# Kernel tuning notes

Measured on AMD Instinct MI355X. Metric: run time of the kernel, lower is better.

Reference implementation:

```python
import jax, jax.numpy as jnp
import numpy as np

T, N, I, H, OUT = 16, 4096, 4, 32, 1


def setup_inputs() -> dict:
    key = jax.random.key(0)
    ks = jax.random.split(key, 12)
    f32 = jnp.float32
    x_path = jax.random.normal(ks[0], (T, N, I), f32)
    adj = jax.random.normal(ks[1], (N, N), f32) / np.float32(np.sqrt(N))
    W_enc = jax.random.normal(ks[2], (I, H), f32) / np.float32(np.sqrt(I))
    b_enc = jnp.zeros((H,), f32)
    W_gcn = jax.random.normal(ks[3], (H, H), f32) / np.float32(np.sqrt(H))
    b_gcn = jnp.zeros((H,), f32)
    W_time = jax.random.normal(ks[4], (H, H), f32) / np.float32(np.sqrt(H))
    b_time = jnp.zeros((H,), f32)
    W_proj = jax.random.normal(ks[5], (H, H * I), f32) * np.float32(0.1 / np.sqrt(H))
    b_proj = jnp.zeros((H * I,), f32)
    W_d1 = jax.random.normal(ks[6], (H, 16), f32) / np.float32(np.sqrt(H))
    b_d1 = jnp.zeros((16,), f32)
    W_d2 = jax.random.normal(ks[7], (16, OUT), f32) / np.float32(4.0)
    b_d2 = jnp.zeros((OUT,), f32)
    return dict(x_path=x_path, adj=adj, W_enc=W_enc, b_enc=b_enc,
                W_gcn=W_gcn, b_gcn=b_gcn, W_time=W_time, b_time=b_time,
                W_proj=W_proj, b_proj=b_proj, W_d1=W_d1, b_d1=b_d1,
                W_d2=W_d2, b_d2=b_d2)


def _natural_cubic_coeffs(y):
    # y: (T, C) samples on uniform grid t=0..T-1 (h=1).
    # Natural cubic spline: tridiagonal solve for second derivatives M.
    Tn = y.shape[0]
    main = jnp.ones((Tn,), y.dtype).at[1:-1].set(4.0)
    A = jnp.diag(main)
    idx = jnp.arange(1, Tn - 1)
    A = A.at[idx, idx - 1].set(1.0).at[idx, idx + 1].set(1.0)
    rhs = jnp.zeros_like(y).at[1:-1].set(6.0 * (y[2:] - 2.0 * y[1:-1] + y[:-2]))
    M = jnp.linalg.solve(A, rhs)
    b = (y[1:] - y[:-1]) - (2.0 * M[:-1] + M[1:]) / 6.0
    c = M[:-1] / 2.0
    d = (M[1:] - M[:-1]) / 6.0
    return b, c, d  # each (T-1, C); dX/dt on interval i at local s: b+2cs+3ds^2


def reference(x_path, adj, W_enc, b_enc, W_gcn, b_gcn, W_time, b_time,
              W_proj, b_proj, W_d1, b_d1, W_d2, b_d2):
    Tn, Nn, In = x_path.shape
    Hn = W_enc.shape[1]
    y = x_path.reshape(Tn, Nn * In)
    sb, sc, sd = _natural_cubic_coeffs(y)

    # z0 = encoder(X(t0)); spline value at grid point 0 equals the sample.
    z0 = x_path[0] @ W_enc + b_enc  # (N, H)

    def vf(z, dxdt):
        # SpatialVectorField + projector + block-diagonal Jacobian applied to dX/dt.
        # z: (N, H), dxdt: (N, I)
        zn = adj @ z                                     # GCN neighbor aggregation
        h = jax.nn.relu(zn @ W_gcn + b_gcn + z @ W_time + b_time)
        sens = (h @ W_proj + b_proj).reshape(Nn, Hn, In)  # per-site Jacobian blocks
        # site_identity * sens -> block-diag; matmul with dX reduces to per-site contraction
        return jnp.einsum('nhi,ni->nh', sens, dxdt)

    def rk4_step(z, coefs):
        bi, ci, di = coefs  # (N*I,)
        def dxdt(s):
            return (bi + 2.0 * ci * s + 3.0 * di * s * s).reshape(Nn, In)
        k1 = vf(z, dxdt(0.0))
        k2 = vf(z + 0.5 * k1, dxdt(0.5))
        k3 = vf(z + 0.5 * k2, dxdt(0.5))
        k4 = vf(z + k3, dxdt(1.0))
        zn = z + (k1 + 2.0 * k2 + 2.0 * k3 + k4) / 6.0
        return zn, zn

    _, zs = jax.lax.scan(rk4_step, z0, (sb, sc, sd))
    zT = jnp.concatenate([z0[None], zs], axis=0)  # (T, N, H)

    hdec = jax.nn.relu(zT @ W_d1 + b_d1)
    return jax.nn.sigmoid(hdec @ W_d2 + b_d2)  # (T, N, OUT)
```

## Files before the change

### kernel.cpp

```cpp
#include <hip/hip_runtime.h>
#include <hip/hip_bf16.h>

#define NN 4096
#define NI 16384
#define HH 32

typedef __attribute__((ext_vector_type(8))) short short8;
typedef __attribute__((ext_vector_type(4))) float f32x4;

__device__ __forceinline__ short f2bs(float f) {
  __hip_bfloat16 b = __float2bfloat16(f);
  return *(short*)&b;
}

__global__ __launch_bounds__(512) void k_cvt(const float* __restrict__ a,
                                             short* __restrict__ ab) {
  const int tid = threadIdx.x;
  const int W = tid >> 6, lane = tid & 63;
  const int fr = lane & 15, oct = lane >> 4;
  const int R = blockIdx.x;
  const float* srow = a + (long)(R * 16 + fr) * NN + W * 512 + oct * 8;
  short* drow = ab + ((long)(R * 8 + W) * 16) * 512 + lane * 8;
#pragma unroll 4
  for (int i = 0; i < 16; ++i) {
    const float4 u0 = *(const float4*)(srow + i * 32);
    const float4 u1 = *(const float4*)(srow + i * 32 + 4);
    short8 r;
    r[0] = f2bs(u0.x); r[1] = f2bs(u0.y); r[2] = f2bs(u0.z); r[3] = f2bs(u0.w);
    r[4] = f2bs(u1.x); r[5] = f2bs(u1.y); r[6] = f2bs(u1.z); r[7] = f2bs(u1.w);
    *(short8*)(drow + i * 512) = r;
  }
}

__device__ __forceinline__ long zt_idx(int n, int h) {
  const int hb = h >> 4, hl = h & 15;
  const int kb = n >> 5, oct = (n >> 3) & 3, j = n & 7;
  return ((long)(hb * 128 + kb) * 64 + hl + 16 * oct) * 8 + j;
}

__global__ void k_spline(const float* __restrict__ x,
                         float* __restrict__ dx0, float* __restrict__ dxh,
                         float* __restrict__ dx1) {
  const int c = blockIdx.x * 256 + threadIdx.x;
  float y[16];
#pragma unroll
  for (int t = 0; t < 16; ++t) y[t] = x[t * NI + c];
  float cp[15], dp[15], M[16];
  cp[1] = 0.25f;
  dp[1] = (6.f * (y[2] - 2.f * y[1] + y[0])) * 0.25f;
#pragma unroll
  for (int i = 2; i <= 14; ++i) {
    float ri = 6.f * (y[i + 1] - 2.f * y[i] + y[i - 1]);
    float inv = 1.f / (4.f - cp[i - 1]);
    cp[i] = inv;
    dp[i] = (ri - dp[i - 1]) * inv;
  }
  M[0] = 0.f; M[15] = 0.f;
  M[14] = dp[14];
#pragma unroll
  for (int i = 13; i >= 1; --i) M[i] = dp[i] - cp[i] * M[i + 1];
#pragma unroll
  for (int i = 0; i < 15; ++i) {
    float b = (y[i + 1] - y[i]) - (2.f * M[i] + M[i + 1]) * (1.f / 6.f);
    float cc = 0.5f * M[i];
    float dd = (M[i + 1] - M[i]) * (1.f / 6.f);
    dx0[i * NI + c] = b;
    dxh[i * NI + c] = b + cc + 0.75f * dd;
    dx1[i * NI + c] = b + 2.f * cc + 3.f * dd;
  }
}

__global__ void k_enc(const float* __restrict__ x,
                      const float* __restrict__ We,
                      const float* __restrict__ be,
                      float* __restrict__ zcur, float* __restrict__ ze,
                      short* __restrict__ zT) {
  const int g = blockIdx.x * 256 + threadIdx.x;
  const int n = g >> 5, h = g & 31;
  float acc = be[h];
#pragma unroll
  for (int i = 0; i < 4; ++i) acc = fmaf(x[n * 4 + i], We[i * 32 + h], acc);
  zcur[g] = acc;
  ze[g] = acc;
  zT[zt_idx(n, h)] = f2bs(acc);
}

__global__ void k_dec0(const float* __restrict__ z,
                       const float* __restrict__ W1,
                       const float* __restrict__ b1,
                       const float* __restrict__ W2,
                       const float* __restrict__ b2,
                       float* __restrict__ out) {
  __shared__ float W1s[32][17];
  __shared__ float b1s[16], W2s[16], b2s;
  const int tid = threadIdx.x;
  for (int idx = tid; idx < 512; idx += 256) W1s[idx >> 4][idx & 15] = W1[idx];
  if (tid < 16) { b1s[tid] = b1[tid]; W2s[tid] = W2[tid]; }
  if (tid == 0) b2s = b2[0];
  __syncthreads();
  const int n = blockIdx.x * 256 + tid;
  const float* zr = z + (long)n * 32;
  float zv[32];
#pragma unroll
  for (int hh = 0; hh < 32; ++hh) zv[hh] = zr[hh];
  float acc = b2s;
#pragma unroll
  for (int jj = 0; jj < 16; ++jj) {
    float hv = b1s[jj];
#pragma unroll
    for (int hh = 0; hh < 32; ++hh) hv = fmaf(zv[hh], W1s[hh][jj], hv);
    acc = fmaf(fmaxf(hv, 0.f), W2s[jj], acc);
  }
  out[n] = 1.f / (1.f + expf(-acc));
}

__global__ __launch_bounds__(1024) void k_vf(
    const short* __restrict__ adjb,
    const short* __restrict__ zT_in,
    short* __restrict__ zT_out,
    float* __restrict__ z_eval,
    const float* __restrict__ z_base,
    float* __restrict__ z_next,
    float* __restrict__ kout,
    const float* __restrict__ k1, const float* __restrict__ k2,
    const float* __restrict__ k3,
    const float* __restrict__ dxsel,
    const float* __restrict__ Wg, const float* __restrict__ bg,
    const float* __restrict__ Wt, const float* __restrict__ bt,
    const float* __restrict__ Wp, const float* __restrict__ bp,
    const float* __restrict__ Wd1, const float* __restrict__ bd1,
    const float* __restrict__ Wd2, const float* __restrict__ bd2,
    float* __restrict__ out, int out_base, int j) {
  __shared__ float red2[16][32][17];
  __shared__ float zn_s[16][33];
  __shared__ float h_s[16][33];
  __shared__ float ze_s[16][33];
  __shared__ float Wg_s[32][32];
  __shared__ float Wt_s[32][32];
  __shared__ float Wp_s[32][136];
  __shared__ float Wd1_s[32][16];
  __shared__ float bgt_s[32];
  __shared__ float bp_s[128];
  __shared__ float dsm[33];

  const int tid = threadIdx.x;
  const int lane = tid & 63;
  const int w = tid >> 6;
  const int r0 = blockIdx.x * 16;
  const int lane8 = lane * 8;

  f32x4 a0 = {0.f,0.f,0.f,0.f}, a1 = {0.f,0.f,0.f,0.f};
  const short* ap  = adjb + ((long)(blockIdx.x * 128 + w * 8)) * 512 + lane8;
  const short* b0p = zT_in + ((long)(w * 8)) * 512 + lane8;
  const short* b1p = zT_in + ((long)(128 + w * 8)) * 512 + lane8;
#pragma unroll
  for (int i = 0; i < 8; ++i) {
    const short8 av = *(const short8*)(ap + i * 512);
    const short8 b0 = *(const short8*)(b0p + i * 512);
    const short8 b1 = *(const short8*)(b1p + i * 512);
    a0 = __builtin_amdgcn_mfma_f32_16x16x32_bf16(av, b0, a0, 0, 0, 0);
    a1 = __builtin_amdgcn_mfma_f32_16x16x32_bf16(av, b1, a1, 0, 0, 0);
  }

  for (int idx = tid; idx < 1024; idx += 1024) { }
  if (tid < 1024) {
    if (tid < 512) {
      Wg_s[tid >> 5][tid & 31] = Wg[tid];
      Wt_s[tid >> 5][tid & 31] = Wt[tid];
    } else {
      const int q = tid - 512;
      Wg_s[(q + 512) >> 5][q & 31] = Wg[512 + q];
      Wt_s[(q + 512) >> 5][q & 31] = Wt[512 + q];
    }
  }
  for (int idx = tid; idx < 4096; idx += 1024)
    Wp_s[idx >> 7][idx & 127] = Wp[idx];
  if (tid < 512) Wd1_s[tid >> 4][tid & 15] = Wd1[tid];
  if (tid < 32) bgt_s[tid] = bg[tid] + bt[tid];
  if (tid < 128) bp_s[tid] = bp[tid];
  if (tid < 512) ze_s[tid >> 5][tid & 31] = z_eval[r0 * 32 + tid];
  if (tid < 16) { dsm[tid] = bd1[tid]; dsm[16 + tid] = Wd2[tid]; }
  if (tid == 0) dsm[32] = bd2[0];

  {
    const int crow = (lane >> 4) * 4;
    const int ccol = lane & 15;
#pragma unroll
    for (int q = 0; q < 4; ++q) {
      red2[crow + q][ccol][w] = a0[q];
      red2[crow + q][ccol + 16][w] = a1[q];
    }
  }
  __syncthreads();

  const int r = (tid >> 5) & 15, c = tid & 31;
  if (tid < 512) {
    float zn = 0.f;
#pragma unroll
    for (int q = 0; q < 16; ++q) zn += red2[r][c][q];
    zn_s[r][c] = zn;
  }
  __syncthreads();

  if (tid < 512) {
    float hv = bgt_s[c];
#pragma unroll
    for (int kk = 0; kk < 32; ++kk)
      hv = fmaf(zn_s[r][kk], Wg_s[kk][c], fmaf(ze_s[r][kk], Wt_s[kk][c], hv));
    h_s[r][c] = fmaxf(hv, 0.f);
  }
  __syncthreads();

  float znew = 0.f;
  if (tid < 512) {
    const int row = r0 + r;
    float hr[32];
#pragma unroll
    for (int hp = 0; hp < 32; ++hp) hr[hp] = h_s[r][hp];
    float s0 = bp_s[c * 4], s1 = bp_s[c * 4 + 1], s2 = bp_s[c * 4 + 2], s3 = bp_s[c * 4 + 3];
#pragma unroll
    for (int hp = 0; hp < 32; ++hp) {
      const float4 wv = *(const float4*)&Wp_s[hp][c * 4];
      s0 = fmaf(hr[hp], wv.x, s0);
      s1 = fmaf(hr[hp], wv.y, s1);
      s2 = fmaf(hr[hp], wv.z, s2);
      s3 = fmaf(hr[hp], wv.w, s3);
    }
    const float4 dxv = *(const float4*)&dxsel[row * 4];
    const float kv = s0 * dxv.x + s1 * dxv.y + s2 * dxv.z + s3 * dxv.w;
    const long g = (long)row * 32 + c;
    if (j == 4) {
      znew = z_base[g] + (k1[g] + 2.f * k2[g] + 2.f * k3[g] + kv) * (1.f / 6.f);
      z_next[g] = znew;
    } else {
      kout[g] = kv;
      znew = z_base[g] + ((j == 3) ? 1.f : 0.5f) * kv;
    }
    z_eval[g] = znew;
    zT_out[zt_idx(row, c)] = f2bs(znew);
  }

  if (j == 4) {
    __syncthreads();
    if (tid < 512) zn_s[r][c] = znew;
    __syncthreads();
    if (tid < 16) {
      float acc = dsm[32];
#pragma unroll
      for (int jj = 0; jj < 16; ++jj) {
        float hv = dsm[jj];
#pragma unroll
        for (int hh = 0; hh < 32; ++hh) hv = fmaf(zn_s[tid][hh], Wd1_s[hh][jj], hv);
        acc = fmaf(fmaxf(hv, 0.f), dsm[16 + jj], acc);
      }
      out[out_base + r0 + tid] = 1.f / (1.f + expf(-acc));
    }
  }
}

extern "C" void kernel_launch(void* const* d_in, const int* in_sizes, int n_in,
                              void* d_out, int out_size, void* d_ws, size_t ws_size,
                              hipStream_t stream) {
  (void)in_sizes; (void)n_in; (void)out_size; (void)ws_size;
  const float* x      = (const float*)d_in[0];
  const float* adj    = (const float*)d_in[1];
  const float* W_enc  = (const float*)d_in[2];
  const float* b_enc  = (const float*)d_in[3];
  const float* W_gcn  = (const float*)d_in[4];
  const float* b_gcn  = (const float*)d_in[5];
  const float* W_time = (const float*)d_in[6];
  const float* b_time = (const float*)d_in[7];
  const float* W_proj = (const float*)d_in[8];
  const float* b_proj = (const float*)d_in[9];
  const float* W_d1   = (const float*)d_in[10];
  const float* b_d1   = (const float*)d_in[11];
  const float* W_d2   = (const float*)d_in[12];
  const float* b_d2   = (const float*)d_in[13];
  float* out = (float*)d_out;

  float* dx0   = (float*)d_ws;
  float* dxh   = dx0 + 15 * NI;
  float* dx1   = dxh + 15 * NI;
  float* zcur  = dx1 + 15 * NI;
  float* znext = zcur + NN * HH;
  float* zev   = znext + NN * HH;
  float* k1b   = zev + NN * HH;
  float* k2b   = k1b + NN * HH;
  float* k3b   = k2b + NN * HH;
  short* zTa   = (short*)(k3b + NN * HH);
  short* zTb   = zTa + HH * NN;
  short* adjb  = zTb + HH * NN;

  k_cvt<<<256, 512, 0, stream>>>(adj, adjb);
  k_spline<<<64, 256, 0, stream>>>(x, dx0, dxh, dx1);
  k_enc<<<512, 256, 0, stream>>>(x, W_enc, b_enc, zcur, zev, zTa);
  k_dec0<<<16, 256, 0, stream>>>(zcur, W_d1, b_d1, W_d2, b_d2, out);

  short* zin = zTa;
  short* zout = zTb;
  for (int t = 0; t < 15; ++t) {
    const float* ds[4] = { dx0 + t * NI, dxh + t * NI, dxh + t * NI, dx1 + t * NI };
    for (int j = 1; j <= 4; ++j) {
      float* ko = (j == 1) ? k1b : (j == 2) ? k2b : k3b;
      k_vf<<<256, 1024, 0, stream>>>(adjb, zin, zout, zev, zcur, znext, ko,
                                     k1b, k2b, k3b, ds[j - 1],
                                     W_gcn, b_gcn, W_time, b_time, W_proj, b_proj,
                                     W_d1, b_d1, W_d2, b_d2, out, (t + 1) * NN, j);
      short* tmp = zin; zin = zout; zout = tmp;
    }
    float* tz = zcur; zcur = znext; znext = tz;
  }
}
```

Measured before the change: 791.7 us.

## Fuse the whole RK4 integration into one persistent cooperative kernel with grid barriers

Replaces the 60 per-stage kernel launches, plus the separate convert, encoder and decoder kernels, with one persistent cooperative kernel. It synchronises the stages with a two-level atomic grid barrier. Each block keeps its bf16 slice of adj in registers, converted once from fp32, and holds z and the k accumulators in shared memory, so global round-trips of z, k1-k3 and the adj re-reads go away. The cost is a grid barrier per stage, higher register pressure from the 8 resident short8 fragments, and reliance on all 256 blocks being co-resident. If the cooperative launch fails, the fallback launch could deadlock.

After: 1.676 ms. 112% more time.

```diff
diff --git a/kernel.cpp b/kernel.cpp
--- a/kernel.cpp
+++ b/kernel.cpp
@@ -11,25 +11,6 @@
 __device__ __forceinline__ short f2bs(float f) {
   __hip_bfloat16 b = __float2bfloat16(f);
   return *(short*)&b;
-}
-
-__global__ __launch_bounds__(512) void k_cvt(const float* __restrict__ a,
-                                             short* __restrict__ ab) {
-  const int tid = threadIdx.x;
-  const int W = tid >> 6, lane = tid & 63;
-  const int fr = lane & 15, oct = lane >> 4;
-  const int R = blockIdx.x;
-  const float* srow = a + (long)(R * 16 + fr) * NN + W * 512 + oct * 8;
-  short* drow = ab + ((long)(R * 8 + W) * 16) * 512 + lane * 8;
-#pragma unroll 4
-  for (int i = 0; i < 16; ++i) {
-    const float4 u0 = *(const float4*)(srow + i * 32);
-    const float4 u1 = *(const float4*)(srow + i * 32 + 4);
-    short8 r;
-    r[0] = f2bs(u0.x); r[1] = f2bs(u0.y); r[2] = f2bs(u0.z); r[3] = f2bs(u0.w);
-    r[4] = f2bs(u1.x); r[5] = f2bs(u1.y); r[6] = f2bs(u1.z); r[7] = f2bs(u1.w);
-    *(short8*)(drow + i * 512) = r;
-  }
 }
 
 __device__ __forceinline__ long zt_idx(int n, int h) {
@@ -40,7 +21,11 @@
 
 __global__ void k_spline(const float* __restrict__ x,
                          float* __restrict__ dx0, float* __restrict__ dxh,
-                         float* __restrict__ dx1) {
+                         float* __restrict__ dx1, unsigned* __restrict__ bar) {
+  if (blockIdx.x == 0) {
+    bar[threadIdx.x] = 0u;
+    if (threadIdx.x < 64) bar[256 + threadIdx.x] = 0u;
+  }
   const int c = blockIdx.x * 256 + threadIdx.x;
   float y[16];
 #pragma unroll
@@ -70,71 +55,61 @@
   }
 }
 
-__global__ void k_enc(const float* __restrict__ x,
-                      const float* __restrict__ We,
-                      const float* __restrict__ be,
-                      float* __restrict__ zcur, float* __restrict__ ze,
-                      short* __restrict__ zT) {
-  const int g = blockIdx.x * 256 + threadIdx.x;
-  const int n = g >> 5, h = g & 31;
-  float acc = be[h];
-#pragma unroll
-  for (int i = 0; i < 4; ++i) acc = fmaf(x[n * 4 + i], We[i * 32 + h], acc);
-  zcur[g] = acc;
-  ze[g] = acc;
-  zT[zt_idx(n, h)] = f2bs(acc);
-}
-
-__global__ void k_dec0(const float* __restrict__ z,
-                       const float* __restrict__ W1,
-                       const float* __restrict__ b1,
-                       const float* __restrict__ W2,
-                       const float* __restrict__ b2,
-                       float* __restrict__ out) {
-  __shared__ float W1s[32][17];
-  __shared__ float b1s[16], W2s[16], b2s;
-  const int tid = threadIdx.x;
-  for (int idx = tid; idx < 512; idx += 256) W1s[idx >> 4][idx & 15] = W1[idx];
-  if (tid < 16) { b1s[tid] = b1[tid]; W2s[tid] = W2[tid]; }
-  if (tid == 0) b2s = b2[0];
+__device__ __forceinline__ void gridbar(unsigned* bar, int bid, int e) {
   __syncthreads();
-  const int n = blockIdx.x * 256 + tid;
-  const float* zr = z + (long)n * 32;
-  float zv[32];
-#pragma unroll
-  for (int hh = 0; hh < 32; ++hh) zv[hh] = zr[hh];
-  float acc = b2s;
-#pragma unroll
-  for (int jj = 0; jj < 16; ++jj) {
-    float hv = b1s[jj];
-#pragma unroll
-    for (int hh = 0; hh < 32; ++hh) hv = fmaf(zv[hh], W1s[hh][jj], hv);
-    acc = fmaf(fmaxf(hv, 0.f), W2s[jj], acc);
-  }
-  out[n] = 1.f / (1.f + expf(-acc));
-}
-
-__global__ __launch_bounds__(1024) void k_vf(
-    const short* __restrict__ adjb,
-    const short* __restrict__ zT_in,
-    short* __restrict__ zT_out,
-    float* __restrict__ z_eval,
-    const float* __restrict__ z_base,
-    float* __restrict__ z_next,
-    float* __restrict__ kout,
-    const float* __restrict__ k1, const float* __restrict__ k2,
-    const float* __restrict__ k3,
-    const float* __restrict__ dxsel,
+  if (threadIdx.x == 0) {
+    __threadfence();
+    unsigned old = __hip_atomic_fetch_add(bar + (bid & 7) * 32, 1u,
+                                          __ATOMIC_RELAXED, __HIP_MEMORY_SCOPE_AGENT);
+    if (old == (unsigned)(32 * e - 1)) {
+      unsigned rr = __hip_atomic_fetch_add(bar + 256, 1u,
+                                           __ATOMIC_RELAXED, __HIP_MEMORY_SCOPE_AGENT);
+      if (rr == (unsigned)(8 * e - 1))
+        __hip_atomic_store(bar + 288, (unsigned)e,
+                           __ATOMIC_RELEASE, __HIP_MEMORY_SCOPE_AGENT);
+    }
+    while (__hip_atomic_load(bar + 288, __ATOMIC_ACQUIRE,
+                             __HIP_MEMORY_SCOPE_AGENT) < (unsigned)e)
+      __builtin_amdgcn_s_sleep(2);
+    __threadfence();
+  }
+  __syncthreads();
+}
+
+__device__ __forceinline__ void dec_block(const float* zsrc ,
+                                          const float* Wd1s ,
+                                          const float* dsm, float* op,
+                                          int r0, int tid) {
+  if (tid < 256) {
+    const int rr = tid >> 4, jj = tid & 15;
+    float hv = dsm[jj];
+#pragma unroll
+    for (int hh = 0; hh < 32; ++hh) hv = fmaf(zsrc[rr * 33 + hh], Wd1s[hh * 16 + jj], hv);
+    float val = fmaxf(hv, 0.f) * dsm[16 + jj];
+#pragma unroll
+    for (int off = 1; off < 16; off <<= 1) val += __shfl_xor(val, off, 64);
+    if (jj == 0) op[r0 + rr] = 1.f / (1.f + expf(-(dsm[32] + val)));
+  }
+}
+
+__global__ __launch_bounds__(1024, 4) void k_ode(
+    const float* __restrict__ adj, const float* __restrict__ x,
+    const float* __restrict__ dx0, const float* __restrict__ dxh,
+    const float* __restrict__ dx1,
+    const float* __restrict__ We, const float* __restrict__ be,
     const float* __restrict__ Wg, const float* __restrict__ bg,
     const float* __restrict__ Wt, const float* __restrict__ bt,
     const float* __restrict__ Wp, const float* __restrict__ bp,
     const float* __restrict__ Wd1, const float* __restrict__ bd1,
     const float* __restrict__ Wd2, const float* __restrict__ bd2,
-    float* __restrict__ out, int out_base, int j) {
+    short* __restrict__ zTa, short* __restrict__ zTb,
+    unsigned* __restrict__ bar, float* __restrict__ out) {
   __shared__ float red2[16][32][17];
   __shared__ float zn_s[16][33];
   __shared__ float h_s[16][33];
   __shared__ float ze_s[16][33];
+  __shared__ float zb_s[16][33];
+  __shared__ float ka_s[16][33];
   __shared__ float Wg_s[32][32];
   __shared__ float Wt_s[32][32];
   __shared__ float Wp_s[32][136];
@@ -146,114 +121,126 @@
   const int tid = threadIdx.x;
   const int lane = tid & 63;
   const int w = tid >> 6;
-  const int r0 = blockIdx.x * 16;
+  const int bid = blockIdx.x;
+  const int r0 = bid * 16;
   const int lane8 = lane * 8;
-
-  f32x4 a0 = {0.f,0.f,0.f,0.f}, a1 = {0.f,0.f,0.f,0.f};
-  const short* ap  = adjb + ((long)(blockIdx.x * 128 + w * 8)) * 512 + lane8;
-  const short* b0p = zT_in + ((long)(w * 8)) * 512 + lane8;
-  const short* b1p = zT_in + ((long)(128 + w * 8)) * 512 + lane8;
-#pragma unroll
-  for (int i = 0; i < 8; ++i) {
-    const short8 av = *(const short8*)(ap + i * 512);
-    const short8 b0 = *(const short8*)(b0p + i * 512);
-    const short8 b1 = *(const short8*)(b1p + i * 512);
-    a0 = __builtin_amdgcn_mfma_f32_16x16x32_bf16(av, b0, a0, 0, 0, 0);
-    a1 = __builtin_amdgcn_mfma_f32_16x16x32_bf16(av, b1, a1, 0, 0, 0);
-  }
-
-  for (int idx = tid; idx < 1024; idx += 1024) { }
-  if (tid < 1024) {
-    if (tid < 512) {
-      Wg_s[tid >> 5][tid & 31] = Wg[tid];
-      Wt_s[tid >> 5][tid & 31] = Wt[tid];
-    } else {
-      const int q = tid - 512;
-      Wg_s[(q + 512) >> 5][q & 31] = Wg[512 + q];
-      Wt_s[(q + 512) >> 5][q & 31] = Wt[512 + q];
+  const int fr = lane & 15, oct = lane >> 4;
+
+  short8 av[8];
+  {
+    const float* arow = adj + (long)(r0 + fr) * NN + w * 256 + oct * 8;
+#pragma unroll
+    for (int i = 0; i < 8; ++i) {
+      const float4 u0 = *(const float4*)(arow + i * 32);
+      const float4 u1 = *(const float4*)(arow + i * 32 + 4);
+      short8 rf;
+      rf[0] = f2bs(u0.x); rf[1] = f2bs(u0.y); rf[2] = f2bs(u0.z); rf[3] = f2bs(u0.w);
+      rf[4] = f2bs(u1.x); rf[5] = f2bs(u1.y); rf[6] = f2bs(u1.z); rf[7] = f2bs(u1.w);
+      av[i] = rf;
     }
   }
+
+  Wg_s[tid >> 5][tid & 31] = Wg[tid];
+  Wt_s[tid >> 5][tid & 31] = Wt[tid];
+#pragma unroll
   for (int idx = tid; idx < 4096; idx += 1024)
     Wp_s[idx >> 7][idx & 127] = Wp[idx];
   if (tid < 512) Wd1_s[tid >> 4][tid & 15] = Wd1[tid];
   if (tid < 32) bgt_s[tid] = bg[tid] + bt[tid];
   if (tid < 128) bp_s[tid] = bp[tid];
-  if (tid < 512) ze_s[tid >> 5][tid & 31] = z_eval[r0 * 32 + tid];
   if (tid < 16) { dsm[tid] = bd1[tid]; dsm[16 + tid] = Wd2[tid]; }
   if (tid == 0) dsm[32] = bd2[0];
 
-  {
-    const int crow = (lane >> 4) * 4;
-    const int ccol = lane & 15;
-#pragma unroll
-    for (int q = 0; q < 4; ++q) {
-      red2[crow + q][ccol][w] = a0[q];
-      red2[crow + q][ccol + 16][w] = a1[q];
-    }
-  }
-  __syncthreads();
-
   const int r = (tid >> 5) & 15, c = tid & 31;
   if (tid < 512) {
-    float zn = 0.f;
-#pragma unroll
-    for (int q = 0; q < 16; ++q) zn += red2[r][c][q];
-    zn_s[r][c] = zn;
+    const int n = r0 + r;
+    float acc = be[c];
+#pragma unroll
+    for (int i = 0; i < 4; ++i) acc = fmaf(x[n * 4 + i], We[i * 32 + c], acc);
+    zb_s[r][c] = acc;
+    ze_s[r][c] = acc;
+    zTa[zt_idx(n, c)] = f2bs(acc);
   }
   __syncthreads();
-
-  if (tid < 512) {
-    float hv = bgt_s[c];
-#pragma unroll
-    for (int kk = 0; kk < 32; ++kk)
-      hv = fmaf(zn_s[r][kk], Wg_s[kk][c], fmaf(ze_s[r][kk], Wt_s[kk][c], hv));
-    h_s[r][c] = fmaxf(hv, 0.f);
-  }
-  __syncthreads();
-
-  float znew = 0.f;
-  if (tid < 512) {
-    const int row = r0 + r;
-    float hr[32];
-#pragma unroll
-    for (int hp = 0; hp < 32; ++hp) hr[hp] = h_s[r][hp];
-    float s0 = bp_s[c * 4], s1 = bp_s[c * 4 + 1], s2 = bp_s[c * 4 + 2], s3 = bp_s[c * 4 + 3];
-#pragma unroll
-    for (int hp = 0; hp < 32; ++hp) {
-      const float4 wv = *(const float4*)&Wp_s[hp][c * 4];
-      s0 = fmaf(hr[hp], wv.x, s0);
-      s1 = fmaf(hr[hp], wv.y, s1);
-      s2 = fmaf(hr[hp], wv.z, s2);
-      s3 = fmaf(hr[hp], wv.w, s3);
-    }
-    const float4 dxv = *(const float4*)&dxsel[row * 4];
-    const float kv = s0 * dxv.x + s1 * dxv.y + s2 * dxv.z + s3 * dxv.w;
-    const long g = (long)row * 32 + c;
-    if (j == 4) {
-      znew = z_base[g] + (k1[g] + 2.f * k2[g] + 2.f * k3[g] + kv) * (1.f / 6.f);
-      z_next[g] = znew;
-    } else {
-      kout[g] = kv;
-      znew = z_base[g] + ((j == 3) ? 1.f : 0.5f) * kv;
-    }
-    z_eval[g] = znew;
-    zT_out[zt_idx(row, c)] = f2bs(znew);
-  }
-
-  if (j == 4) {
-    __syncthreads();
-    if (tid < 512) zn_s[r][c] = znew;
-    __syncthreads();
-    if (tid < 16) {
-      float acc = dsm[32];
-#pragma unroll
-      for (int jj = 0; jj < 16; ++jj) {
-        float hv = dsm[jj];
-#pragma unroll
-        for (int hh = 0; hh < 32; ++hh) hv = fmaf(zn_s[tid][hh], Wd1_s[hh][jj], hv);
-        acc = fmaf(fmaxf(hv, 0.f), dsm[16 + jj], acc);
-      }
-      out[out_base + r0 + tid] = 1.f / (1.f + expf(-acc));
+  dec_block(&zb_s[0][0], &Wd1_s[0][0], dsm, out, r0, tid);
+
+  int ep = 0;
+  gridbar(bar, bid, ++ep);
+
+  const short* zi = zTa;
+  short* zo = zTb;
+
+  for (int t = 0; t < 15; ++t) {
+    const float* dt0 = dx0 + t * NI;
+    const float* dth = dxh + t * NI;
+    const float* dt1 = dx1 + t * NI;
+    for (int j = 1; j <= 4; ++j) {
+      const float* dxp = (j == 1) ? dt0 : (j == 4) ? dt1 : dth;
+
+      f32x4 a0 = {0.f, 0.f, 0.f, 0.f}, a1 = {0.f, 0.f, 0.f, 0.f};
+      const short* bp0 = zi + (w * 8) * 512 + lane8;
+#pragma unroll
+      for (int i = 0; i < 8; ++i) {
+        const short8 b0 = *(const short8*)(bp0 + i * 512);
+        const short8 b1 = *(const short8*)(bp0 + 65536 + i * 512);
+        a0 = __builtin_amdgcn_mfma_f32_16x16x32_bf16(av[i], b0, a0, 0, 0, 0);
+        a1 = __builtin_amdgcn_mfma_f32_16x16x32_bf16(av[i], b1, a1, 0, 0, 0);
+      }
+      {
+        const int crow = (lane >> 4) * 4, ccol = lane & 15;
+#pragma unroll
+        for (int q = 0; q < 4; ++q) {
+          red2[crow + q][ccol][w] = a0[q];
+          red2[crow + q][ccol + 16][w] = a1[q];
+        }
+      }
+      __syncthreads();
+
+      if (tid < 512) {
+        float zn = 0.f;
+#pragma unroll
+        for (int q = 0; q < 16; ++q) zn += red2[r][c][q];
+        zn_s[r][c] = zn;
+      }
+      __syncthreads();
+
+      if (tid < 512) {
+        float hv = bgt_s[c];
+#pragma unroll
+        for (int kk = 0; kk < 32; ++kk)
+          hv = fmaf(zn_s[r][kk], Wg_s[kk][c], fmaf(ze_s[r][kk], Wt_s[kk][c], hv));
+        h_s[r][c] = fmaxf(hv, 0.f);
+      }
+      __syncthreads();
+
+      if (tid < 512) {
+        float s0 = bp_s[c * 4], s1 = bp_s[c * 4 + 1];
+        float s2 = bp_s[c * 4 + 2], s3 = bp_s[c * 4 + 3];
+#pragma unroll
+        for (int hp = 0; hp < 32; ++hp) {
+          const float4 wv = *(const float4*)&Wp_s[hp][c * 4];
+          const float hr = h_s[r][hp];
+          s0 = fmaf(hr, wv.x, s0);
+          s1 = fmaf(hr, wv.y, s1);
+          s2 = fmaf(hr, wv.z, s2);
+          s3 = fmaf(hr, wv.w, s3);
+        }
+        const float4 dxv = *(const float4*)(dxp + (long)(r0 + r) * 4);
+        const float kv = s0 * dxv.x + s1 * dxv.y + s2 * dxv.z + s3 * dxv.w;
+        float zev;
+        if (j == 1)      { ka_s[r][c] = kv;            zev = zb_s[r][c] + 0.5f * kv; }
+        else if (j == 2) { ka_s[r][c] += 2.f * kv;     zev = zb_s[r][c] + 0.5f * kv; }
+        else if (j == 3) { ka_s[r][c] += 2.f * kv;     zev = zb_s[r][c] + kv; }
+        else { zev = zb_s[r][c] + (ka_s[r][c] + kv) * (1.f / 6.f); zb_s[r][c] = zev; }
+        ze_s[r][c] = zev;
+        zo[zt_idx(r0 + r, c)] = f2bs(zev);
+      }
+      if (j == 4) {
+        __syncthreads();
+        dec_block(&zb_s[0][0], &Wd1_s[0][0], dsm, out + (t + 1) * NN, r0, tid);
+      }
+      gridbar(bar, bid, ++ep);
+      const short* tz = zi; zi = zo; zo = (short*)tz;
     }
   }
 }
@@ -278,36 +265,25 @@
   const float* b_d2   = (const float*)d_in[13];
   float* out = (float*)d_out;
 
-  float* dx0   = (float*)d_ws;
-  float* dxh   = dx0 + 15 * NI;
-  float* dx1   = dxh + 15 * NI;
-  float* zcur  = dx1 + 15 * NI;
-  float* znext = zcur + NN * HH;
-  float* zev   = znext + NN * HH;
-  float* k1b   = zev + NN * HH;
-  float* k2b   = k1b + NN * HH;
-  float* k3b   = k2b + NN * HH;
-  short* zTa   = (short*)(k3b + NN * HH);
-  short* zTb   = zTa + HH * NN;
-  short* adjb  = zTb + HH * NN;
-
-  k_cvt<<<256, 512, 0, stream>>>(adj, adjb);
-  k_spline<<<64, 256, 0, stream>>>(x, dx0, dxh, dx1);
-  k_enc<<<512, 256, 0, stream>>>(x, W_enc, b_enc, zcur, zev, zTa);
-  k_dec0<<<16, 256, 0, stream>>>(zcur, W_d1, b_d1, W_d2, b_d2, out);
-
-  short* zin = zTa;
-  short* zout = zTb;
-  for (int t = 0; t < 15; ++t) {
-    const float* ds[4] = { dx0 + t * NI, dxh + t * NI, dxh + t * NI, dx1 + t * NI };
-    for (int j = 1; j <= 4; ++j) {
-      float* ko = (j == 1) ? k1b : (j == 2) ? k2b : k3b;
-      k_vf<<<256, 1024, 0, stream>>>(adjb, zin, zout, zev, zcur, znext, ko,
-                                     k1b, k2b, k3b, ds[j - 1],
-                                     W_gcn, b_gcn, W_time, b_time, W_proj, b_proj,
-                                     W_d1, b_d1, W_d2, b_d2, out, (t + 1) * NN, j);
-      short* tmp = zin; zin = zout; zout = tmp;
-    }
-    float* tz = zcur; zcur = znext; znext = tz;
-  }
-}
+  float* dx0 = (float*)d_ws;
+  float* dxh = dx0 + 15 * NI;
+  float* dx1 = dxh + 15 * NI;
+  short* zTa = (short*)(dx1 + 15 * NI);
+  short* zTb = zTa + HH * NN;
+  unsigned* bar = (unsigned*)(zTb + HH * NN);
+
+  k_spline<<<64, 256, 0, stream>>>(x, dx0, dxh, dx1, bar);
+
+  void* args[] = {(void*)&adj, (void*)&x, (void*)&dx0, (void*)&dxh, (void*)&dx1,
+                  (void*)&W_enc, (void*)&b_enc, (void*)&W_gcn, (void*)&b_gcn,
+                  (void*)&W_time, (void*)&b_time, (void*)&W_proj, (void*)&b_proj,
+                  (void*)&W_d1, (void*)&b_d1, (void*)&W_d2, (void*)&b_d2,
+                  (void*)&zTa, (void*)&zTb, (void*)&bar, (void*)&out};
+  hipError_t err = hipLaunchCooperativeKernel((const void*)k_ode, dim3(256),
+                                              dim3(1024), args, 0, stream);
+  if (err != hipSuccess) {
+    k_ode<<<256, 1024, 0, stream>>>(adj, x, dx0, dxh, dx1, W_enc, b_enc,
+                                    W_gcn, b_gcn, W_time, b_time, W_proj, b_proj,
+                                    W_d1, b_d1, W_d2, b_d2, zTa, zTb, bar, out);
+  }
+}
```
